# Performance work log

Hardware: AMD Instinct MI355X
Metric: run time of the kernel (lower is better)

The kernel has to match this reference:

```python
import jax, jax.numpy as jnp
import numpy as np

SEQ, BATCH, INP = 20, 16384, 2
HID, EMB = 256, 64
TARGET_LEN = 30


def setup_inputs() -> dict:
    key = jax.random.key(0)
    ks = jax.random.split(key, 12)
    s = 0.1
    return {
        "x_input": jax.random.normal(ks[0], (SEQ, BATCH, INP), dtype=jnp.float32),
        # encoder embedding Linear(input_size -> emb_dim)
        "W_emb": jax.random.normal(ks[1], (EMB, INP), dtype=jnp.float32) * s,
        "b_emb": jax.random.normal(ks[2], (EMB,), dtype=jnp.float32) * s,
        # encoder LSTM (input EMB -> hidden HID), PyTorch gate order i,f,g,o; bias = b_ih + b_hh
        "W_ih_enc": jax.random.normal(ks[3], (4 * HID, EMB), dtype=jnp.float32) * s,
        "W_hh_enc": jax.random.normal(ks[4], (4 * HID, HID), dtype=jnp.float32) * s,
        "b_enc": jax.random.normal(ks[5], (4 * HID,), dtype=jnp.float32) * s,
        # decoder LSTM (input INP -> hidden HID)
        "W_ih_dec": jax.random.normal(ks[6], (4 * HID, INP), dtype=jnp.float32) * s,
        "W_hh_dec": jax.random.normal(ks[7], (4 * HID, HID), dtype=jnp.float32) * s,
        "b_dec": jax.random.normal(ks[8], (4 * HID,), dtype=jnp.float32) * s,
        # decoder output Linear(hidden -> input_size)
        "W_out": jax.random.normal(ks[9], (INP, HID), dtype=jnp.float32) * s,
        "b_out": jax.random.normal(ks[10], (INP,), dtype=jnp.float32) * s,
        "target_len": TARGET_LEN,
    }


def _lstm_cell(x, h, c, W_ih, W_hh, b):
    # x: [B, in], h/c: [B, H]; PyTorch gate order: input, forget, cell(g), output
    gates = x @ W_ih.T + h @ W_hh.T + b  # [B, 4H]
    i, f, g, o = jnp.split(gates, 4, axis=-1)
    c_new = jax.nn.sigmoid(f) * c + jax.nn.sigmoid(i) * jnp.tanh(g)
    h_new = jax.nn.sigmoid(o) * jnp.tanh(c_new)
    return h_new, c_new


def reference(x_input, W_emb, b_emb, W_ih_enc, W_hh_enc, b_enc,
              W_ih_dec, W_hh_dec, b_dec, W_out, b_out, target_len):
    B = x_input.shape[1]
    # --- encoder ---
    x_emb = x_input @ W_emb.T + b_emb  # [S, B, EMB]
    h0 = jnp.zeros((B, HID), dtype=x_input.dtype)
    c0 = jnp.zeros((B, HID), dtype=x_input.dtype)

    def enc_step(carry, xt):
        h, c = carry
        h, c = _lstm_cell(xt, h, c, W_ih_enc, W_hh_enc, b_enc)
        return (h, c), None

    (h_enc, c_enc), _ = jax.lax.scan(enc_step, (h0, c0), x_emb)

    dec_in0 = x_input[-1]  # [B, INP]

    def dec_step(carry, _):
        di, h, c = carry
        h, c = _lstm_cell(di, h, c, W_ih_dec, W_hh_dec, b_dec)
        out = h @ W_out.T + b_out  # [B, INP]
        return (out, h, c), out

    _, outputs = jax.lax.scan(dec_step, (dec_in0, h_enc, c_enc), None,
                              length=int(target_len))
    return outputs  # [target_len, B, INP]
```

## Files before the change

### kernel.cpp

```cpp
#include <hip/hip_runtime.h>


#define SEQ  20
#define TLEN 30
#define LOG2E  1.442695041f
#define LOG2E2 2.885390082f

typedef _Float16 half8   __attribute__((ext_vector_type(8)));
typedef _Float16 half4   __attribute__((ext_vector_type(4)));
typedef float    floatx4 __attribute__((ext_vector_type(4)));

__device__ _Float16 g_w_enc[1024 * 288];
__device__ _Float16 g_w_dec0[1024 * 288];
__device__ _Float16 g_w_deff[1024 * 288];
__device__ _Float16 g_wout[512];

__global__ void prep_kernel(const float* __restrict__ W_emb,
                            const float* __restrict__ b_emb,
                            const float* __restrict__ W_ih_enc,
                            const float* __restrict__ W_hh_enc,
                            const float* __restrict__ b_enc,
                            const float* __restrict__ W_ih_dec,
                            const float* __restrict__ W_hh_dec,
                            const float* __restrict__ b_dec,
                            const float* __restrict__ W_out,
                            const float* __restrict__ b_out) {
    int gid = blockIdx.x * blockDim.x + threadIdx.x;
    int stride = gridDim.x * blockDim.x;
    for (int s = gid; s < 1024 * 288; s += stride) {
        int n = s / 288, k = s - n * 288;
        int g = n >> 8, c = (n >> 4) & 15, l16 = n & 15;
        int w = c >> 1, cc = c & 1;
        int i = cc * 4 + g;
        int kt = k >> 5, q = (k >> 3) & 3, j = k & 7;
        int dst = ((w * 9 + kt) * 8 + i) * 512 + q * 128 + l16 * 8 + j;
        float sc = (g == 2) ? LOG2E2 : LOG2E;
        float fe = 0.f, fd = 0.f, ff = 0.f;
        if (k < 256) {
            fe = W_hh_enc[n * 256 + k];
            fd = W_hh_dec[n * 256 + k];
            ff = fd + W_ih_dec[2 * n] * W_out[k]
                    + W_ih_dec[2 * n + 1] * W_out[256 + k];
        } else {
            int kp = k - 256;
            if (kp < 2) {
                fd = W_ih_dec[2 * n + kp];
                const float* wr = &W_ih_enc[n * 64];
                for (int e = 0; e < 64; e++) fe = fmaf(wr[e], W_emb[2 * e + kp], fe);
            } else if (kp == 2) {
                fd = b_dec[n];
                ff = b_dec[n] + W_ih_dec[2 * n] * b_out[0]
                              + W_ih_dec[2 * n + 1] * b_out[1];
                fe = b_enc[n];
                const float* wr = &W_ih_enc[n * 64];
                for (int e = 0; e < 64; e++) fe = fmaf(wr[e], b_emb[e], fe);
            }
        }
        g_w_enc[dst]  = (_Float16)(fe * sc);
        g_w_dec0[dst] = (_Float16)(fd * sc);
        g_w_deff[dst] = (_Float16)(ff * sc);
    }
    if (gid < 512) g_wout[gid] = (_Float16)W_out[gid];
}

__global__ __launch_bounds__(512, 2) void lstm_fused(
        const float* __restrict__ x_input,
        const float* __restrict__ b_out,
        float* __restrict__ out)
{
    __shared__ __align__(16) _Float16 h_pack[2][18432];
    __shared__ __align__(16) float    partial_lds[2][8 * 132];

    const int tid = threadIdx.x;
    const int w   = tid >> 6;
    const int L   = tid & 63;
    const int l16 = L & 15;
    const int q   = L >> 4;
    const long row0 = (long)blockIdx.x * 64;

    {
        int* hz = (int*)&h_pack[0][0];
        for (int idx = tid; idx < 18432; idx += 512) hz[idx] = 0;
    }
    __syncthreads();
    if (tid < 128) {
        int buf = tid >> 6, b = tid & 63;
        h_pack[buf][((b >> 4) * 9 + 8) * 512 + (b & 15) * 8 + 2] = (_Float16)1.f;
    }
    if (tid < 128) {
        int b = tid >> 1, jj = tid & 1;
        h_pack[0][((b >> 4) * 9 + 8) * 512 + (b & 15) * 8 + jj] =
            (_Float16)x_input[(row0 + b) * 2 + jj];
    }

    const float bo = b_out[tid & 1];
    const int aoff = q * 128 + l16 * 8;
    const _Float16* __restrict__ wenc_w  = &g_w_enc[w * 36864];
    const _Float16* __restrict__ wdec0_w = &g_w_dec0[w * 36864];
    const _Float16* __restrict__ wdeff_w = &g_w_deff[w * 36864];

    _Float16 wo[2][2][4];
#pragma unroll
    for (int jj = 0; jj < 2; jj++)
#pragma unroll
        for (int cc = 0; cc < 2; cc++)
#pragma unroll
            for (int r = 0; r < 4; r++)
                wo[jj][cc][r] = g_wout[jj * 256 + 32 * w + 16 * cc + 4 * q + r];

    floatx4 acc[8][4];
    float   c_st[4][2][4];
#pragma unroll
    for (int nt = 0; nt < 4; nt++)
#pragma unroll
        for (int cc = 0; cc < 2; cc++)
#pragma unroll
            for (int r = 0; r < 4; r++) c_st[nt][cc][r] = 0.f;

    __syncthreads();

    int cur = 0;
#pragma unroll 1
    for (int t = 0; t < SEQ + TLEN; t++) {
        const _Float16* __restrict__ Wb =
            (t < SEQ) ? wenc_w : (t == SEQ) ? wdec0_w : wdeff_w;
        const _Float16* __restrict__ hp = h_pack[cur];
        _Float16* __restrict__ hn = h_pack[cur ^ 1];

#pragma unroll
        for (int kt = 0; kt < 9; kt++) {
            half8 B[4];
#pragma unroll
            for (int nt = 0; nt < 4; nt++)
                B[nt] = *(const half8*)&hp[(nt * 9 + kt) * 512 + aoff];
#pragma unroll
            for (int i = 0; i < 8; i++) {
                half8 Aw = *(const half8*)&Wb[(kt * 8 + i) * 512 + aoff];
                if (kt == 0) {
#pragma unroll
                    for (int nt = 0; nt < 4; nt++)
                        acc[i][nt] = __builtin_amdgcn_mfma_f32_16x16x32_f16(
                            Aw, B[nt], (floatx4)(0.f), 0, 0, 0);
                } else {
#pragma unroll
                    for (int nt = 0; nt < 4; nt++)
                        acc[i][nt] = __builtin_amdgcn_mfma_f32_16x16x32_f16(
                            Aw, B[nt], acc[i][nt], 0, 0, 0);
                }
            }
        }

        float xval = 0.f;
        if (t < SEQ && tid < 128) {
            int srct = (t + 1 < SEQ) ? t + 1 : SEQ - 1;
            xval = x_input[(long)srct * 32768 + (row0 + (tid >> 1)) * 2 + (tid & 1)];
        }

        const bool dec = (t >= SEQ);
        float po[4][2];
#pragma unroll
        for (int nt = 0; nt < 4; nt++) { po[nt][0] = 0.f; po[nt][1] = 0.f; }

#pragma unroll
        for (int nt = 0; nt < 4; nt++)
#pragma unroll
            for (int cc = 0; cc < 2; cc++) {
                half4 hv4;
                float hvf[4];
#pragma unroll
                for (int r = 0; r < 4; r++) {
                    float ai = acc[cc * 4 + 0][nt][r];
                    float af = acc[cc * 4 + 1][nt][r];
                    float ag = acc[cc * 4 + 2][nt][r];
                    float ao = acc[cc * 4 + 3][nt][r];
                    float eI = __builtin_amdgcn_exp2f(-ai);
                    float eF = __builtin_amdgcn_exp2f(-af);
                    float eG = __builtin_amdgcn_exp2f(-ag);
                    float eO = __builtin_amdgcn_exp2f(-ao);
                    float a1 = 1.f + eI;
                    float a2 = 1.f + eG;
                    float a3 = 1.f + eF;
                    float t1 = a1 * a2;
                    float num = fmaf(c_st[nt][cc][r], t1, (1.f - eG) * a3);
                    float cn  = num * __builtin_amdgcn_rcpf(t1 * a3);
                    c_st[nt][cc][r] = cn;
                    float cnc = fminf(fmaxf(cn, -12.f), 12.f);
                    float eC = __builtin_amdgcn_exp2f(-LOG2E2 * cnc);
                    float hv = (1.f - eC) *
                        __builtin_amdgcn_rcpf((1.f + eO) * (1.f + eC));
                    hvf[r] = hv;
                    hv4[r] = (_Float16)hv;
                }
                *(half4*)&hn[(nt * 9 + w) * 512 + (2 * cc + (q >> 1)) * 128 +
                             l16 * 8 + 4 * (q & 1)] = hv4;
                if (dec) {
#pragma unroll
                    for (int r = 0; r < 4; r++) {
                        po[nt][0] = fmaf(hvf[r], (float)wo[0][cc][r], po[nt][0]);
                        po[nt][1] = fmaf(hvf[r], (float)wo[1][cc][r], po[nt][1]);
                    }
                }
            }

        if (dec) {
#pragma unroll
            for (int nt = 0; nt < 4; nt++)
#pragma unroll
                for (int jj = 0; jj < 2; jj++) {
                    float s = po[nt][jj];
                    s += __shfl_xor(s, 16);
                    s += __shfl_xor(s, 32);
                    po[nt][jj] = s;
                }
            if (q == 0) {
                float* pl = &partial_lds[t & 1][w * 132];
#pragma unroll
                for (int nt = 0; nt < 4; nt++) {
                    pl[nt * 16 + l16]      = po[nt][0];
                    pl[66 + nt * 16 + l16] = po[nt][1];
                }
            }
        }

        if (t < SEQ && tid < 128) {
            int b = tid >> 1, jj = tid & 1;
            hn[((b >> 4) * 9 + 8) * 512 + (b & 15) * 8 + jj] = (_Float16)xval;
        }

        __syncthreads();

        if (dec && tid < 128) {
            int m = tid >> 1, jj = tid & 1;
            const float* pl = &partial_lds[t & 1][jj * 66 + m];
            float s = bo;
#pragma unroll
            for (int w8 = 0; w8 < 8; w8++) s += pl[w8 * 132];
            out[(long)(t - SEQ) * 32768 + (row0 + m) * 2 + jj] = s;
        }

        cur ^= 1;
    }
}

extern "C" void kernel_launch(void* const* d_in, const int* in_sizes, int n_in,
                              void* d_out, int out_size, void* d_ws, size_t ws_size,
                              hipStream_t stream) {
    (void)in_sizes; (void)n_in; (void)d_ws; (void)ws_size; (void)out_size;
    const float* x      = (const float*)d_in[0];
    const float* W_emb  = (const float*)d_in[1];
    const float* b_emb  = (const float*)d_in[2];
    const float* W_ih_e = (const float*)d_in[3];
    const float* W_hh_e = (const float*)d_in[4];
    const float* b_enc  = (const float*)d_in[5];
    const float* W_ih_d = (const float*)d_in[6];
    const float* W_hh_d = (const float*)d_in[7];
    const float* b_dec  = (const float*)d_in[8];
    const float* W_out  = (const float*)d_in[9];
    const float* b_out  = (const float*)d_in[10];
    float* outp = (float*)d_out;

    prep_kernel<<<512, 256, 0, stream>>>(W_emb, b_emb, W_ih_e, W_hh_e, b_enc,
                                         W_ih_d, W_hh_d, b_dec, W_out, b_out);
    lstm_fused<<<256, 512, 0, stream>>>(x, b_out, outp);
}
```

Baseline: 590.8 us.

## Split MFMA and gate math into halves with staggered order across waves

Splits each step's matrix work into two halves, each followed by its own elementwise gate pass. Waves 0-3 and 4-7 run the halves in opposite order so one group's MFMA work can overlap the other's transcendental math on the same CU. The B operands are now loaded twice from LDS per step, and the cell-state clamp drops its upper bound. The split may also lower live accumulator pressure, but it roughly doubles the shared-memory reads of h.

Result: faster. 572.9 us (-3.0%).

```diff
diff --git a/kernel.cpp b/kernel.cpp
--- a/kernel.cpp
+++ b/kernel.cpp
@@ -63,6 +63,84 @@
     if (gid < 512) g_wout[gid] = (_Float16)W_out[gid];
 }
 
+template<int I0>
+__device__ __forceinline__ void mfma_pass(
+        const _Float16* __restrict__ Wb,
+        const _Float16* __restrict__ hp,
+        int aoff, floatx4 (&acc)[8][4])
+{
+#pragma unroll
+    for (int kt = 0; kt < 9; kt++) {
+        half8 B[4];
+#pragma unroll
+        for (int nt = 0; nt < 4; nt++)
+            B[nt] = *(const half8*)&hp[(nt * 9 + kt) * 512 + aoff];
+#pragma unroll
+        for (int ii = 0; ii < 4; ii++) {
+            const int i = I0 + ii;
+            half8 Aw = *(const half8*)&Wb[(kt * 8 + i) * 512 + aoff];
+            if (kt == 0) {
+#pragma unroll
+                for (int nt = 0; nt < 4; nt++)
+                    acc[i][nt] = __builtin_amdgcn_mfma_f32_16x16x32_f16(
+                        Aw, B[nt], (floatx4)(0.f), 0, 0, 0);
+            } else {
+#pragma unroll
+                for (int nt = 0; nt < 4; nt++)
+                    acc[i][nt] = __builtin_amdgcn_mfma_f32_16x16x32_f16(
+                        Aw, B[nt], acc[i][nt], 0, 0, 0);
+            }
+        }
+    }
+}
+
+template<int CC>
+__device__ __forceinline__ void ew_half(
+        floatx4 (&acc)[8][4], float (&c_st)[4][2][4],
+        float (&po)[4][2], const _Float16 (&wo)[2][2][4],
+        _Float16* __restrict__ hn, bool dec,
+        int w, int q, int l16)
+{
+#pragma unroll
+    for (int nt = 0; nt < 4; nt++) {
+        half4 hv4;
+        float hvf[4];
+#pragma unroll
+        for (int r = 0; r < 4; r++) {
+            float ai = acc[CC * 4 + 0][nt][r];
+            float af = acc[CC * 4 + 1][nt][r];
+            float ag = acc[CC * 4 + 2][nt][r];
+            float ao = acc[CC * 4 + 3][nt][r];
+            float eI = __builtin_amdgcn_exp2f(-ai);
+            float eF = __builtin_amdgcn_exp2f(-af);
+            float eG = __builtin_amdgcn_exp2f(-ag);
+            float eO = __builtin_amdgcn_exp2f(-ao);
+            float a1 = 1.f + eI;
+            float a2 = 1.f + eG;
+            float a3 = 1.f + eF;
+            float t1 = a1 * a2;
+            float num = fmaf(c_st[nt][CC][r], t1, (1.f - eG) * a3);
+            float cn  = num * __builtin_amdgcn_rcpf(t1 * a3);
+            c_st[nt][CC][r] = cn;
+            float cnc = fmaxf(cn, -12.f);
+            float eC = __builtin_amdgcn_exp2f(-LOG2E2 * cnc);
+            float hv = (1.f - eC) *
+                __builtin_amdgcn_rcpf((1.f + eO) * (1.f + eC));
+            hvf[r] = hv;
+            hv4[r] = (_Float16)hv;
+        }
+        *(half4*)&hn[(nt * 9 + w) * 512 + (2 * CC + (q >> 1)) * 128 +
+                     l16 * 8 + 4 * (q & 1)] = hv4;
+        if (dec) {
+#pragma unroll
+            for (int r = 0; r < 4; r++) {
+                po[nt][0] = fmaf(hvf[r], (float)wo[0][CC][r], po[nt][0]);
+                po[nt][1] = fmaf(hvf[r], (float)wo[1][CC][r], po[nt][1]);
+            }
+        }
+    }
+}
+
 __global__ __launch_bounds__(512, 2) void lstm_fused(
         const float* __restrict__ x_input,
         const float* __restrict__ b_out,
@@ -77,6 +155,7 @@
     const int l16 = L & 15;
     const int q   = L >> 4;
     const long row0 = (long)blockIdx.x * 64;
+    const bool par = ((w >> 2) & 1) != 0;
 
     {
         int* hz = (int*)&h_pack[0][0];
@@ -126,29 +205,7 @@
             (t < SEQ) ? wenc_w : (t == SEQ) ? wdec0_w : wdeff_w;
         const _Float16* __restrict__ hp = h_pack[cur];
         _Float16* __restrict__ hn = h_pack[cur ^ 1];
-
-#pragma unroll
-        for (int kt = 0; kt < 9; kt++) {
-            half8 B[4];
-#pragma unroll
-            for (int nt = 0; nt < 4; nt++)
-                B[nt] = *(const half8*)&hp[(nt * 9 + kt) * 512 + aoff];
-#pragma unroll
-            for (int i = 0; i < 8; i++) {
-                half8 Aw = *(const half8*)&Wb[(kt * 8 + i) * 512 + aoff];
-                if (kt == 0) {
-#pragma unroll
-                    for (int nt = 0; nt < 4; nt++)
-                        acc[i][nt] = __builtin_amdgcn_mfma_f32_16x16x32_f16(
-                            Aw, B[nt], (floatx4)(0.f), 0, 0, 0);
-                } else {
-#pragma unroll
-                    for (int nt = 0; nt < 4; nt++)
-                        acc[i][nt] = __builtin_amdgcn_mfma_f32_16x16x32_f16(
-                            Aw, B[nt], acc[i][nt], 0, 0, 0);
-                }
-            }
-        }
+        const bool dec = (t >= SEQ);
 
         float xval = 0.f;
         if (t < SEQ && tid < 128) {
@@ -156,51 +213,21 @@
             xval = x_input[(long)srct * 32768 + (row0 + (tid >> 1)) * 2 + (tid & 1)];
         }
 
-        const bool dec = (t >= SEQ);
         float po[4][2];
 #pragma unroll
         for (int nt = 0; nt < 4; nt++) { po[nt][0] = 0.f; po[nt][1] = 0.f; }
 
-#pragma unroll
-        for (int nt = 0; nt < 4; nt++)
-#pragma unroll
-            for (int cc = 0; cc < 2; cc++) {
-                half4 hv4;
-                float hvf[4];
-#pragma unroll
-                for (int r = 0; r < 4; r++) {
-                    float ai = acc[cc * 4 + 0][nt][r];
-                    float af = acc[cc * 4 + 1][nt][r];
-                    float ag = acc[cc * 4 + 2][nt][r];
-                    float ao = acc[cc * 4 + 3][nt][r];
-                    float eI = __builtin_amdgcn_exp2f(-ai);
-                    float eF = __builtin_amdgcn_exp2f(-af);
-                    float eG = __builtin_amdgcn_exp2f(-ag);
-                    float eO = __builtin_amdgcn_exp2f(-ao);
-                    float a1 = 1.f + eI;
-                    float a2 = 1.f + eG;
-                    float a3 = 1.f + eF;
-                    float t1 = a1 * a2;
-                    float num = fmaf(c_st[nt][cc][r], t1, (1.f - eG) * a3);
-                    float cn  = num * __builtin_amdgcn_rcpf(t1 * a3);
-                    c_st[nt][cc][r] = cn;
-                    float cnc = fminf(fmaxf(cn, -12.f), 12.f);
-                    float eC = __builtin_amdgcn_exp2f(-LOG2E2 * cnc);
-                    float hv = (1.f - eC) *
-                        __builtin_amdgcn_rcpf((1.f + eO) * (1.f + eC));
-                    hvf[r] = hv;
-                    hv4[r] = (_Float16)hv;
-                }
-                *(half4*)&hn[(nt * 9 + w) * 512 + (2 * cc + (q >> 1)) * 128 +
-                             l16 * 8 + 4 * (q & 1)] = hv4;
-                if (dec) {
-#pragma unroll
-                    for (int r = 0; r < 4; r++) {
-                        po[nt][0] = fmaf(hvf[r], (float)wo[0][cc][r], po[nt][0]);
-                        po[nt][1] = fmaf(hvf[r], (float)wo[1][cc][r], po[nt][1]);
-                    }
-                }
-            }
+        if (!par) {
+            mfma_pass<0>(Wb, hp, aoff, acc);
+            ew_half<0>(acc, c_st, po, wo, hn, dec, w, q, l16);
+            mfma_pass<4>(Wb, hp, aoff, acc);
+            ew_half<1>(acc, c_st, po, wo, hn, dec, w, q, l16);
+        } else {
+            mfma_pass<4>(Wb, hp, aoff, acc);
+            ew_half<1>(acc, c_st, po, wo, hn, dec, w, q, l16);
+            mfma_pass<0>(Wb, hp, aoff, acc);
+            ew_half<0>(acc, c_st, po, wo, hn, dec, w, q, l16);
+        }
 
         if (dec) {
 #pragma unroll
```
